# Optimization experiments

Hardware: AMD Instinct MI355X
Metric: run time of the kernel (lower is better)

The kernel has to match this reference:

```python
import jax, jax.numpy as jnp
import numpy as np

B, T, D = 4, 50, 512
SRC, SENTS, WORDS = 400, 16, 40
NEG = jnp.float32(-1e30)  # stands in for -inf mask fill (numerically identical post-softmax)


def _seq_mask(lengths, max_len):
    # [n, max_len] bool, True where position < length
    return jnp.arange(max_len)[None, :] < lengths[:, None]


def _mlp_score(q, h, Wq, bq, Uc, v):
    # Bahdanau additive score: v^T tanh(W q + U h)
    # q: [b,t,d], h: [b,s,d] -> [b,t,s]
    wq = q @ Wq + bq                       # [b,t,d]
    uh = h @ Uc                            # [b,s,d]
    wquh = jnp.tanh(wq[:, :, None, :] + uh[:, None, :, :])  # [b,t,s,d]
    return jnp.einsum('btsd,d->bts', wquh, v)


def setup_inputs() -> dict:
    key = jax.random.key(0)
    ks = jax.random.split(key, 20)
    s = np.float32(1.0 / np.sqrt(D))
    def p(k, shape):
        return jax.random.normal(k, shape, jnp.float32) * s
    return {
        'source': jax.random.normal(ks[0], (B, T, D), jnp.float32),
        'src_bank': jax.random.normal(ks[1], (SRC, B, D), jnp.float32),
        'src_lengths': jax.random.randint(ks[2], (B,), 1, SRC + 1),
        'qa_sent_bank': jax.random.normal(ks[3], (SENTS, B, D), jnp.float32),
        'qa_sent_lengths': jax.random.randint(ks[4], (B,), 1, SENTS + 1),
        'qa_word_bank': jax.random.normal(ks[5], (WORDS, B, SENTS, D), jnp.float32),
        'qa_word_lengths': jax.random.randint(ks[6], (B, SENTS), 1, WORDS + 1),
        'Wq_word': p(ks[7], (D, D)), 'bq_word': jnp.zeros((D,), jnp.float32),
        'Uc_word': p(ks[8], (D, D)), 'v_word': p(ks[9], (D,)),
        'Wq_sent': p(ks[10], (D, D)), 'bq_sent': jnp.zeros((D,), jnp.float32),
        'Uc_sent': p(ks[11], (D, D)), 'v_sent': p(ks[12], (D,)),
        'Wq_pass': p(ks[13], (D, D)), 'bq_pass': jnp.zeros((D,), jnp.float32),
        'Uc_pass': p(ks[14], (D, D)), 'v_pass': p(ks[15], (D,)),
    }


def _forward(source, src_bank, qa_sent_bank, qa_word_bank,
             Wq_word, bq_word, Uc_word, v_word,
             Wq_sent, bq_sent, Uc_sent, v_sent,
             Wq_pass, bq_pass, Uc_pass, v_pass,
             src_lengths, qa_word_lengths):
    b = source.shape[0]
    # [words,b,sents,d] -> [b,sents,words,d] -> [b, sents*words, d]
    qa_word = jnp.transpose(qa_word_bank, (1, 2, 0, 3)).reshape(b, SENTS * WORDS, D)
    src = jnp.transpose(src_bank, (1, 0, 2))       # [b,src,d]
    sent = jnp.transpose(qa_sent_bank, (1, 0, 2))  # [b,sents,d]

    qa_word_align = _mlp_score(source, qa_word, Wq_word, bq_word, Uc_word, v_word)  # [b,t,sents*words]
    src_align = _mlp_score(source, src, Wq_pass, bq_pass, Uc_pass, v_pass)          # [b,t,src]
    qa_sent_align = _mlp_score(source, sent, Wq_sent, bq_sent, Uc_sent, v_sent)     # [b,t,sents]

    # hierarchical combination: word score scaled by its sentence score
    qa_hier = (qa_word_align.reshape(b, T, SENTS, WORDS)
               * qa_sent_align[..., None]).reshape(b, T, SENTS * WORDS)

    align = jnp.concatenate([src_align, qa_hier], axis=-1)  # [b,t,src+sents*words]

    qa_mask = _seq_mask(qa_word_lengths.reshape(-1), WORDS).reshape(b, SENTS * WORDS)[:, None, :]
    src_mask = _seq_mask(src_lengths, SRC)[:, None, :]
    mask = jnp.concatenate([src_mask, qa_mask], axis=-1)

    align = jnp.where(mask, align, NEG)
    align_vectors = jax.nn.softmax(align, axis=-1)  # joint length-masked softmax

    memory = jnp.concatenate([src, qa_word], axis=1)          # [b, src+sents*words, d]
    c = jnp.einsum('bts,bsd->btd', align_vectors, memory)     # weighted context sum
    return c


def reference(source, src_bank, src_lengths, qa_sent_bank, qa_sent_lengths,
              qa_word_bank, qa_word_lengths,
              Wq_word, bq_word, Uc_word, v_word,
              Wq_sent, bq_sent, Uc_sent, v_sent,
              Wq_pass, bq_pass, Uc_pass, v_pass):
    # qa_sent_lengths is accepted but unused, matching the original forward()
    return _forward(source, src_bank, qa_sent_bank, qa_word_bank,
                    Wq_word, bq_word, Uc_word, v_word,
                    Wq_sent, bq_sent, Uc_sent, v_sent,
                    Wq_pass, bq_pass, Uc_pass, v_pass,
                    src_lengths, qa_word_lengths)
```

## Files before the change

### kernel.cpp

```cpp
#include <hip/hip_runtime.h>
#include <hip/hip_bf16.h>


#define B_    4
#define T_    50
#define D_    512
#define SRC_  400
#define SENTS_ 16
#define WORDS_ 40
#define NW_   640
#define NMEM_ 1040
#define NK_   1056
#define NJOB_ 1056

#define C2L2E 2.8853900817779268f

typedef unsigned short ushort_t;
using s8v = __attribute__((ext_vector_type(8))) short;
using f4v = __attribute__((ext_vector_type(4))) float;

#define OFF_WQ_WORD 0
#define OFF_WQ_SENT 102400
#define OFF_WQ_PASS 204800
#define OFF_UH_SRC  307200
#define OFF_UH_WORD 1126400
#define OFF_UH_SENT 2437120
#define OFF_SC_SRC  2469888
#define OFF_SC_WORD 2549888
#define OFF_SC_SENT 2677888
#define P_BYTE_OFF  10724352ull
#define MT_BYTE_OFF 11265024ull
#define WT_BYTE_OFF 15590400ull

__device__ __forceinline__ ushort_t f2b(float f) {
    __hip_bfloat16 h = __float2bfloat16(f);
    return *(ushort_t*)&h;
}

__global__ __launch_bounds__(256) void k0f_transpose(
    const float* __restrict__ w0, const float* __restrict__ w1,
    const float* __restrict__ w2, const float* __restrict__ w3,
    const float* __restrict__ w4, const float* __restrict__ w5,
    const float* __restrict__ src_bank, const float* __restrict__ qa_word_bank,
    ushort_t* __restrict__ wt, ushort_t* __restrict__ mt)
{
    __shared__ float tile[32][33];
    int bid = blockIdx.x;
    int tx = threadIdx.x & 31, ty = threadIdx.x >> 5;
    if (bid < 1536) {
        int z = bid >> 8, r = bid & 255;
        int n0 = (r & 15) * 32, k0 = (r >> 4) * 32;
        const float* W;
        switch (z) {
            case 0: W = w0; break; case 1: W = w1; break; case 2: W = w2; break;
            case 3: W = w3; break; case 4: W = w4; break; default: W = w5; break;
        }
        ushort_t* Wt = wt + z * (D_ * D_);
#pragma unroll
        for (int a = 0; a < 4; ++a)
            tile[ty + a * 8][tx] = W[(k0 + ty + a * 8) * D_ + n0 + tx];
        __syncthreads();
#pragma unroll
        for (int a = 0; a < 4; ++a)
            Wt[(n0 + ty + a * 8) * D_ + k0 + tx] = f2b(tile[tx][ty + a * 8]);
    } else {
        int tb = bid - 1536;
        int b = tb / 528, r = tb - b * 528;
        int s0 = (r % 33) * 32, d0 = (r / 33) * 32;
#pragma unroll
        for (int a = 0; a < 4; ++a) {
            int s = s0 + ty + a * 8;
            float val = 0.f;
            if (s < SRC_) {
                val = src_bank[(s * B_ + b) * D_ + d0 + tx];
            } else if (s < NMEM_) {
                int j = s - SRC_; int se = j / WORDS_; int wd = j - se * WORDS_;
                val = qa_word_bank[((wd * B_ + b) * SENTS_ + se) * D_ + d0 + tx];
            }
            tile[ty + a * 8][tx] = val;
        }
        __syncthreads();
        ushort_t* base = mt + (size_t)b * D_ * NK_;
#pragma unroll
        for (int a = 0; a < 4; ++a) {
            int d = d0 + ty + a * 8;
            base[(size_t)d * NK_ + s0 + tx] = f2b(tile[tx][ty + a * 8]);
        }
    }
}

__global__ __launch_bounds__(256) void k1_gemm(
    const float* __restrict__ source, const float* __restrict__ src_bank,
    const float* __restrict__ qa_sent_bank, const float* __restrict__ qa_word_bank,
    const ushort_t* __restrict__ wt,
    const float* __restrict__ bq_word, const float* __restrict__ bq_sent,
    const float* __restrict__ bq_pass,
    float* __restrict__ wsf)
{
    __shared__ short At[64 * 32];
    __shared__ short Bt[64 * 32];
    int bid = blockIdx.x;
    int z, rem;
    if (bid < 96)       { z = bid >> 5; rem = bid & 31; }
    else if (bid < 416) { z = 3; rem = bid - 96; }
    else if (bid < 616) { z = 4; rem = bid - 416; }
    else                { z = 5; rem = bid - 616; }
    int by = rem >> 3, bx = rem & 7;
    int M, atype; const float* bias; float* C;
    switch (z) {
        case 0: M = 200;  atype = 0; bias = bq_word; C = wsf + OFF_WQ_WORD; break;
        case 1: M = 200;  atype = 0; bias = bq_sent; C = wsf + OFF_WQ_SENT; break;
        case 2: M = 200;  atype = 0; bias = bq_pass; C = wsf + OFF_WQ_PASS; break;
        case 3: M = 2560; atype = 1; bias = nullptr; C = wsf + OFF_UH_WORD; break;
        case 4: M = 1600; atype = 2; bias = nullptr; C = wsf + OFF_UH_SRC;  break;
        default: M = 64;  atype = 3; bias = nullptr; C = wsf + OFF_UH_SENT; break;
    }
    int m0 = by * 64, n0 = bx * 64;
    const ushort_t* W = wt + z * (D_ * D_);

    int tid = threadIdx.x;
    int lane = tid & 63, wv = tid >> 6;
    int quad = lane >> 4, l16 = lane & 15;
    int sm = tid >> 2, koff = (tid & 3) * 8;

    const float* arow = nullptr;
    {
        int r = m0 + sm;
        if (r < M) {
            if (atype == 0) arow = source + r * D_;
            else if (atype == 1) { int b = r / NW_; int j = r - b * NW_;
                                   int se = j / WORDS_; int wd = j - se * WORDS_;
                                   arow = qa_word_bank + ((wd * B_ + b) * SENTS_ + se) * D_; }
            else if (atype == 2) { int b = r / SRC_; int j = r - b * SRC_;
                                   arow = src_bank + (j * B_ + b) * D_; }
            else                 { int b = r >> 4; int s2 = r & 15;
                                   arow = qa_sent_bank + (s2 * B_ + b) * D_; }
        }
    }
    const ushort_t* wrow = W + (n0 + sm) * D_;

    auto loadA = [&](float* r, int kk) {
        if (arow) {
            float4 f0 = *(const float4*)(arow + kk * 32 + koff);
            float4 f1 = *(const float4*)(arow + kk * 32 + koff + 4);
            r[0]=f0.x; r[1]=f0.y; r[2]=f0.z; r[3]=f0.w;
            r[4]=f1.x; r[5]=f1.y; r[6]=f1.z; r[7]=f1.w;
        } else {
#pragma unroll
            for (int i = 0; i < 8; ++i) r[i] = 0.f;
        }
    };

    f4v acc[4] = { {0.f,0.f,0.f,0.f}, {0.f,0.f,0.f,0.f},
                   {0.f,0.f,0.f,0.f}, {0.f,0.f,0.f,0.f} };

    float a0[8], a1[8];
    int4 w0v, w1v;
    loadA(a0, 0); w0v = *(const int4*)(wrow + 0 * 32 + koff);
    loadA(a1, 1); w1v = *(const int4*)(wrow + 1 * 32 + koff);

    for (int kk = 0; kk < 16; ++kk) {
        union { ushort_t u[8]; int4 v; } pk;
#pragma unroll
        for (int i = 0; i < 8; ++i) pk.u[i] = f2b(a0[i]);
        *(int4*)(At + sm * 32 + koff) = pk.v;
        *(int4*)(Bt + sm * 32 + koff) = w0v;
        __syncthreads();
#pragma unroll
        for (int i = 0; i < 8; ++i) a0[i] = a1[i];
        w0v = w1v;
        if (kk < 14) {
            loadA(a1, kk + 2);
            w1v = *(const int4*)(wrow + (kk + 2) * 32 + koff);
        }
        s8v af = *(const s8v*)(At + (wv * 16 + l16) * 32 + quad * 8);
#pragma unroll
        for (int ng = 0; ng < 4; ++ng) {
            s8v bf = *(const s8v*)(Bt + (ng * 16 + l16) * 32 + quad * 8);
            acc[ng] = __builtin_amdgcn_mfma_f32_16x16x32_bf16(af, bf, acc[ng], 0, 0, 0);
        }
        __syncthreads();
    }
#pragma unroll
    for (int ng = 0; ng < 4; ++ng) {
        int col = n0 + ng * 16 + l16;
        float bb = bias ? bias[col] : 0.f;
#pragma unroll
        for (int rr = 0; rr < 4; ++rr) {
            int row = m0 + wv * 16 + quad * 4 + rr;
            if (row < M) C[row * D_ + col] = (acc[ng][rr] + bb) * C2L2E;
        }
    }
}

__global__ __launch_bounds__(256) void k2_scores(
    const float* __restrict__ v_word, const float* __restrict__ v_sent,
    const float* __restrict__ v_pass,
    const int* __restrict__ src_lengths, const int* __restrict__ qa_word_lengths,
    float* __restrict__ wsf)
{
    int lane = threadIdx.x & 63;
    int jid = blockIdx.x * 4 + (threadIdx.x >> 6);
    int job = jid / 5, fifth = jid - job * 5;
    int b = job / NJOB_, slot = job - b * NJOB_;
    const float* uh; const float* v; const float* wq; float* out; int ostride;
    if (slot < SRC_) {
        if (slot >= src_lengths[b]) return;
        uh = wsf + OFF_UH_SRC + (size_t)(b * SRC_ + slot) * D_;
        v = v_pass; wq = wsf + OFF_WQ_PASS + b * T_ * D_;
        out = wsf + OFF_SC_SRC + b * T_ * SRC_ + slot; ostride = SRC_;
    } else if (slot < NMEM_) {
        int j = slot - SRC_;
        int se = j / WORDS_; int wd = j - se * WORDS_;
        if (wd >= qa_word_lengths[b * SENTS_ + se]) return;
        uh = wsf + OFF_UH_WORD + (size_t)(b * NW_ + j) * D_;
        v = v_word; wq = wsf + OFF_WQ_WORD + b * T_ * D_;
        out = wsf + OFF_SC_WORD + b * T_ * NW_ + j; ostride = NW_;
    } else {
        int s2 = slot - NMEM_;
        uh = wsf + OFF_UH_SENT + (size_t)(b * SENTS_ + s2) * D_;
        v = v_sent; wq = wsf + OFF_WQ_SENT + b * T_ * D_;
        out = wsf + OFF_SC_SENT + b * T_ * SENTS_ + s2; ostride = SENTS_;
    }
    int d0 = lane * 8;
    float4 u0 = *(const float4*)(uh + d0);
    float4 u1 = *(const float4*)(uh + d0 + 4);
    float uhr[8] = {u0.x, u0.y, u0.z, u0.w, u1.x, u1.y, u1.z, u1.w};
    float4 v0 = *(const float4*)(v + d0);
    float4 v1 = *(const float4*)(v + d0 + 4);
    float vr[8] = {v0.x, v0.y, v0.z, v0.w, v1.x, v1.y, v1.z, v1.w};

    float vs = ((vr[0] + vr[1]) + (vr[2] + vr[3])) + ((vr[4] + vr[5]) + (vr[6] + vr[7]));
#pragma unroll
    for (int off = 32; off > 0; off >>= 1) vs += __shfl_xor(vs, off, 64);

    const float* wqh = wq + (fifth * 10) * D_ + d0;
    int tbase = fifth * 10;
#pragma unroll 1
    for (int g = 0; g < 2; ++g) {
        float a5[5];
#pragma unroll
        for (int u5 = 0; u5 < 5; ++u5) {
            const float* wr = wqh + (g * 5 + u5) * D_;
            float4 w0 = *(const float4*)(wr);
            float4 w1 = *(const float4*)(wr + 4);
            float wrr[8] = {w0.x, w0.y, w0.z, w0.w, w1.x, w1.y, w1.z, w1.w};
            float a = 0.f;
#pragma unroll
            for (int j = 0; j < 8; ++j) {
                float e = __builtin_amdgcn_exp2f(wrr[j] + uhr[j]);
                float r = __builtin_amdgcn_rcpf(e + 1.f);
                a = fmaf(vr[j], r, a);
            }
            a5[u5] = a;
        }
#pragma unroll
        for (int off = 32; off > 0; off >>= 1) {
#pragma unroll
            for (int u5 = 0; u5 < 5; ++u5) a5[u5] += __shfl_xor(a5[u5], off, 64);
        }
        if (lane == 0) {
#pragma unroll
            for (int u5 = 0; u5 < 5; ++u5)
                out[(tbase + g * 5 + u5) * ostride] = fmaf(-2.f, a5[u5], vs);
        }
    }
}

__global__ __launch_bounds__(256) void k3a_softmax(
    const int* __restrict__ src_lengths, const int* __restrict__ qa_word_lengths,
    const float* __restrict__ wsf, ushort_t* __restrict__ P)
{
    __shared__ float p[NMEM_];
    __shared__ float red[4];
    int tid = threadIdx.x, lane = tid & 63, wv = tid >> 6;
    int bt = blockIdx.x, b = bt / T_, t = bt - b * T_;
    const float* sc_src  = wsf + OFF_SC_SRC  + bt * SRC_;
    const float* sc_word = wsf + OFF_SC_WORD + bt * NW_;
    const float* sc_sent = wsf + OFF_SC_SENT + bt * SENTS_;
    int slen = src_lengths[b];
    float mx = -3.0e38f;
    for (int j = tid; j < NMEM_; j += 256) {
        float val;
        if (j < SRC_) {
            val = (j < slen) ? sc_src[j] : -1e30f;
        } else {
            int jj = j - SRC_; int se = jj / WORDS_; int wd = jj - se * WORDS_;
            float raw = sc_word[jj] * sc_sent[se];
            val = (wd < qa_word_lengths[b * SENTS_ + se]) ? raw : -1e30f;
        }
        p[j] = val;
        mx = fmaxf(mx, val);
    }
#pragma unroll
    for (int off = 32; off > 0; off >>= 1) mx = fmaxf(mx, __shfl_xor(mx, off, 64));
    if (lane == 0) red[wv] = mx;
    __syncthreads();
    mx = fmaxf(fmaxf(red[0], red[1]), fmaxf(red[2], red[3]));
    __syncthreads();
    float lsum = 0.f;
    for (int j = tid; j < NMEM_; j += 256) {
        float e = __expf(p[j] - mx);
        p[j] = e; lsum += e;
    }
#pragma unroll
    for (int off = 32; off > 0; off >>= 1) lsum += __shfl_xor(lsum, off, 64);
    if (lane == 0) red[wv] = lsum;
    __syncthreads();
    float inv = 1.f / (red[0] + red[1] + red[2] + red[3]);
    ushort_t* prow = P + (size_t)(b * 64 + t) * NK_;
    for (int j = tid; j < NK_; j += 256)
        prow[j] = (j < NMEM_) ? f2b(p[j] * inv) : (ushort_t)0;
}

__global__ __launch_bounds__(256) void k3c_gemm(
    const ushort_t* __restrict__ P, const ushort_t* __restrict__ Mt,
    float* __restrict__ out)
{
    __shared__ short At[64 * 32];
    __shared__ short Bt[32 * 32];
    int b = blockIdx.y;
    int n0 = blockIdx.x * 32;
    int tid = threadIdx.x;
    int lane = tid & 63, wv = tid >> 6;
    int quad = lane >> 4, l16 = lane & 15;
    int smA = tid >> 2, koffA = (tid & 3) * 8;
    int smB = tid >> 3, koffB = (tid & 7) * 4;

    const ushort_t* arow = P + (size_t)(b * 64 + smA) * NK_ + koffA;
    const ushort_t* brow = Mt + ((size_t)(b * D_ + n0 + smB)) * NK_ + koffB;

    f4v acc[2] = { {0.f,0.f,0.f,0.f}, {0.f,0.f,0.f,0.f} };

    int4 a0 = *(const int4*)(arow);
    int2 b0 = *(const int2*)(brow);
    int4 a1 = *(const int4*)(arow + 32);
    int2 b1 = *(const int2*)(brow + 32);
    int4 a2 = *(const int4*)(arow + 64);
    int2 b2 = *(const int2*)(brow + 64);

    for (int kk = 0; kk < 33; ++kk) {
        *(int4*)(At + smA * 32 + koffA) = a0;
        *(int2*)(Bt + smB * 32 + koffB) = b0;
        __syncthreads();
        a0 = a1; a1 = a2; b0 = b1; b1 = b2;
        if (kk < 30) {
            a2 = *(const int4*)(arow + (kk + 3) * 32);
            b2 = *(const int2*)(brow + (kk + 3) * 32);
        }
        s8v af = *(const s8v*)(At + (wv * 16 + l16) * 32 + quad * 8);
#pragma unroll
        for (int ng = 0; ng < 2; ++ng) {
            s8v bf = *(const s8v*)(Bt + (ng * 16 + l16) * 32 + quad * 8);
            acc[ng] = __builtin_amdgcn_mfma_f32_16x16x32_bf16(af, bf, acc[ng], 0, 0, 0);
        }
        __syncthreads();
    }
#pragma unroll
    for (int ng = 0; ng < 2; ++ng) {
        int col = n0 + ng * 16 + l16;
#pragma unroll
        for (int rr = 0; rr < 4; ++rr) {
            int row = wv * 16 + quad * 4 + rr;
            if (row < T_) out[(size_t)(b * T_ + row) * D_ + col] = acc[ng][rr];
        }
    }
}

extern "C" void kernel_launch(void* const* d_in, const int* in_sizes, int n_in,
                              void* d_out, int out_size, void* d_ws, size_t ws_size,
                              hipStream_t stream)
{
    (void)in_sizes; (void)n_in; (void)out_size; (void)ws_size;
    const float* source          = (const float*)d_in[0];
    const float* src_bank        = (const float*)d_in[1];
    const int*   src_lengths     = (const int*)d_in[2];
    const float* qa_sent_bank    = (const float*)d_in[3];
    const float* qa_word_bank    = (const float*)d_in[5];
    const int*   qa_word_lengths = (const int*)d_in[6];
    const float* Wq_word = (const float*)d_in[7];
    const float* bq_word = (const float*)d_in[8];
    const float* Uc_word = (const float*)d_in[9];
    const float* v_word  = (const float*)d_in[10];
    const float* Wq_sent = (const float*)d_in[11];
    const float* bq_sent = (const float*)d_in[12];
    const float* Uc_sent = (const float*)d_in[13];
    const float* v_sent  = (const float*)d_in[14];
    const float* Wq_pass = (const float*)d_in[15];
    const float* bq_pass = (const float*)d_in[16];
    const float* Uc_pass = (const float*)d_in[17];
    const float* v_pass  = (const float*)d_in[18];

    float* wsf = (float*)d_ws;
    ushort_t* Pb  = (ushort_t*)((char*)d_ws + P_BYTE_OFF);
    ushort_t* mt  = (ushort_t*)((char*)d_ws + MT_BYTE_OFF);
    ushort_t* wt  = (ushort_t*)((char*)d_ws + WT_BYTE_OFF);
    float* out = (float*)d_out;

    k0f_transpose<<<dim3(3648), dim3(256), 0, stream>>>(
        Wq_word, Wq_sent, Wq_pass, Uc_word, Uc_pass, Uc_sent,
        src_bank, qa_word_bank, wt, mt);
    k1_gemm<<<dim3(624), dim3(256), 0, stream>>>(
        source, src_bank, qa_sent_bank, qa_word_bank, wt,
        bq_word, bq_sent, bq_pass, wsf);
    k2_scores<<<dim3(5280), dim3(256), 0, stream>>>(
        v_word, v_sent, v_pass, src_lengths, qa_word_lengths, wsf);
    k3a_softmax<<<dim3(200), dim3(256), 0, stream>>>(src_lengths, qa_word_lengths, wsf, Pb);
    k3c_gemm<<<dim3(16, 4), dim3(256), 0, stream>>>(Pb, mt, out);
}
```

Baseline: 153.0 us.

## Fuse weight transpose into projection GEMM and merge with memory transpose kernel

```diff
diff --git a/kernel.cpp b/kernel.cpp
--- a/kernel.cpp
+++ b/kernel.cpp
@@ -30,43 +30,32 @@
 #define OFF_SC_SENT 2677888
 #define P_BYTE_OFF  10724352ull
 #define MT_BYTE_OFF 11265024ull
-#define WT_BYTE_OFF 15590400ull
 
 __device__ __forceinline__ ushort_t f2b(float f) {
     __hip_bfloat16 h = __float2bfloat16(f);
     return *(ushort_t*)&h;
 }
 
-__global__ __launch_bounds__(256) void k0f_transpose(
+__global__ __launch_bounds__(256) void kA(
+    const float* __restrict__ source, const float* __restrict__ src_bank,
+    const float* __restrict__ qa_sent_bank, const float* __restrict__ qa_word_bank,
     const float* __restrict__ w0, const float* __restrict__ w1,
     const float* __restrict__ w2, const float* __restrict__ w3,
     const float* __restrict__ w4, const float* __restrict__ w5,
-    const float* __restrict__ src_bank, const float* __restrict__ qa_word_bank,
-    ushort_t* __restrict__ wt, ushort_t* __restrict__ mt)
+    const float* __restrict__ bq_word, const float* __restrict__ bq_sent,
+    const float* __restrict__ bq_pass,
+    float* __restrict__ wsf, ushort_t* __restrict__ mt)
 {
-    __shared__ float tile[32][33];
+    __shared__ float smemf[4224];
     int bid = blockIdx.x;
-    int tx = threadIdx.x & 31, ty = threadIdx.x >> 5;
-    if (bid < 1536) {
-        int z = bid >> 8, r = bid & 255;
-        int n0 = (r & 15) * 32, k0 = (r >> 4) * 32;
-        const float* W;
-        switch (z) {
-            case 0: W = w0; break; case 1: W = w1; break; case 2: W = w2; break;
-            case 3: W = w3; break; case 4: W = w4; break; default: W = w5; break;
-        }
-        ushort_t* Wt = wt + z * (D_ * D_);
-#pragma unroll
-        for (int a = 0; a < 4; ++a)
-            tile[ty + a * 8][tx] = W[(k0 + ty + a * 8) * D_ + n0 + tx];
-        __syncthreads();
-#pragma unroll
-        for (int a = 0; a < 4; ++a)
-            Wt[(n0 + ty + a * 8) * D_ + k0 + tx] = f2b(tile[tx][ty + a * 8]);
-    } else {
-        int tb = bid - 1536;
+    int tid = threadIdx.x;
+
+    if (bid >= 624) {
+        int tb = bid - 624;
         int b = tb / 528, r = tb - b * 528;
         int s0 = (r % 33) * 32, d0 = (r / 33) * 32;
+        float (*tile)[33] = (float(*)[33])smemf;
+        int tx = tid & 31, ty = tid >> 5;
 #pragma unroll
         for (int a = 0; a < 4; ++a) {
             int s = s0 + ty + a * 8;
@@ -86,58 +75,52 @@
             int d = d0 + ty + a * 8;
             base[(size_t)d * NK_ + s0 + tx] = f2b(tile[tx][ty + a * 8]);
         }
-    }
-}
-
-__global__ __launch_bounds__(256) void k1_gemm(
-    const float* __restrict__ source, const float* __restrict__ src_bank,
-    const float* __restrict__ qa_sent_bank, const float* __restrict__ qa_word_bank,
-    const ushort_t* __restrict__ wt,
-    const float* __restrict__ bq_word, const float* __restrict__ bq_sent,
-    const float* __restrict__ bq_pass,
-    float* __restrict__ wsf)
-{
-    __shared__ short At[64 * 32];
-    __shared__ short Bt[64 * 32];
-    int bid = blockIdx.x;
+        return;
+    }
+
     int z, rem;
     if (bid < 96)       { z = bid >> 5; rem = bid & 31; }
     else if (bid < 416) { z = 3; rem = bid - 96; }
     else if (bid < 616) { z = 4; rem = bid - 416; }
     else                { z = 5; rem = bid - 616; }
     int by = rem >> 3, bx = rem & 7;
-    int M, atype; const float* bias; float* C;
+    int M, atype; const float* bias; const float* W; float* C;
     switch (z) {
-        case 0: M = 200;  atype = 0; bias = bq_word; C = wsf + OFF_WQ_WORD; break;
-        case 1: M = 200;  atype = 0; bias = bq_sent; C = wsf + OFF_WQ_SENT; break;
-        case 2: M = 200;  atype = 0; bias = bq_pass; C = wsf + OFF_WQ_PASS; break;
-        case 3: M = 2560; atype = 1; bias = nullptr; C = wsf + OFF_UH_WORD; break;
-        case 4: M = 1600; atype = 2; bias = nullptr; C = wsf + OFF_UH_SRC;  break;
-        default: M = 64;  atype = 3; bias = nullptr; C = wsf + OFF_UH_SENT; break;
+        case 0: M = 200;  atype = 0; bias = bq_word; W = w0; C = wsf + OFF_WQ_WORD; break;
+        case 1: M = 200;  atype = 0; bias = bq_sent; W = w1; C = wsf + OFF_WQ_SENT; break;
+        case 2: M = 200;  atype = 0; bias = bq_pass; W = w2; C = wsf + OFF_WQ_PASS; break;
+        case 3: M = 2560; atype = 1; bias = nullptr; W = w3; C = wsf + OFF_UH_WORD; break;
+        case 4: M = 1600; atype = 2; bias = nullptr; W = w4; C = wsf + OFF_UH_SRC;  break;
+        default: M = 64;  atype = 3; bias = nullptr; W = w5; C = wsf + OFF_UH_SENT; break;
     }
     int m0 = by * 64, n0 = bx * 64;
-    const ushort_t* W = wt + z * (D_ * D_);
-
-    int tid = threadIdx.x;
-    int lane = tid & 63, wv = tid >> 6;
-    int quad = lane >> 4, l16 = lane & 15;
+
+    int lane = tid & 63, wvx = tid >> 6, quad = lane >> 4, l16 = lane & 15;
     int sm = tid >> 2, koff = (tid & 3) * 8;
+    int rW = tid >> 3, cW = (tid & 7) * 8;
+    int rWs = rW * 68 + (cW ^ (((rW >> 3) & 3) << 4));
+    int nB = tid >> 2, kB8 = (tid & 3) * 8;
+    int colp = nB ^ (((kB8 >> 3) & 3) << 4);
+
+    short* At = (short*)smemf;
+    short* Bt = (short*)(smemf + 1024);
+    float* Wtmp = smemf + 2048;
 
     const float* arow = nullptr;
     {
-        int r = m0 + sm;
-        if (r < M) {
-            if (atype == 0) arow = source + r * D_;
-            else if (atype == 1) { int b = r / NW_; int j = r - b * NW_;
+        int rr = m0 + sm;
+        if (rr < M) {
+            if (atype == 0) arow = source + rr * D_;
+            else if (atype == 1) { int b = rr / NW_; int j = rr - b * NW_;
                                    int se = j / WORDS_; int wd = j - se * WORDS_;
                                    arow = qa_word_bank + ((wd * B_ + b) * SENTS_ + se) * D_; }
-            else if (atype == 2) { int b = r / SRC_; int j = r - b * SRC_;
+            else if (atype == 2) { int b = rr / SRC_; int j = rr - b * SRC_;
                                    arow = src_bank + (j * B_ + b) * D_; }
-            else                 { int b = r >> 4; int s2 = r & 15;
+            else                 { int b = rr >> 4; int s2 = rr & 15;
                                    arow = qa_sent_bank + (s2 * B_ + b) * D_; }
         }
     }
-    const ushort_t* wrow = W + (n0 + sm) * D_;
+    const float* wbase = W + n0 + cW;
 
     auto loadA = [&](float* r, int kk) {
         if (arow) {
@@ -150,30 +133,56 @@
             for (int i = 0; i < 8; ++i) r[i] = 0.f;
         }
     };
+    auto loadW = [&](float* r, int kk) {
+        const float* p = wbase + (kk * 32 + rW) * D_;
+        float4 f0 = *(const float4*)p;
+        float4 f1 = *(const float4*)(p + 4);
+        r[0]=f0.x; r[1]=f0.y; r[2]=f0.z; r[3]=f0.w;
+        r[4]=f1.x; r[5]=f1.y; r[6]=f1.z; r[7]=f1.w;
+    };
+    auto storeWtmp = [&](const float* r) {
+        *(float4*)(Wtmp + rWs)     = float4{r[0], r[1], r[2], r[3]};
+        *(float4*)(Wtmp + rWs + 4) = float4{r[4], r[5], r[6], r[7]};
+    };
+    auto storeAt = [&](const float* r) {
+        union { ushort_t u[8]; int4 v; } pk;
+#pragma unroll
+        for (int i = 0; i < 8; ++i) pk.u[i] = f2b(r[i]);
+        *(int4*)(At + sm * 32 + koff) = pk.v;
+    };
+    auto buildBt = [&]() {
+        union { ushort_t u[8]; int4 v; } pk;
+#pragma unroll
+        for (int i = 0; i < 8; ++i) pk.u[i] = f2b(Wtmp[(kB8 + i) * 68 + colp]);
+        *(int4*)(Bt + nB * 32 + kB8) = pk.v;
+    };
 
     f4v acc[4] = { {0.f,0.f,0.f,0.f}, {0.f,0.f,0.f,0.f},
                    {0.f,0.f,0.f,0.f}, {0.f,0.f,0.f,0.f} };
 
-    float a0[8], a1[8];
-    int4 w0v, w1v;
-    loadA(a0, 0); w0v = *(const int4*)(wrow + 0 * 32 + koff);
-    loadA(a1, 1); w1v = *(const int4*)(wrow + 1 * 32 + koff);
+    float ac[8], an[8], wn[8];
+    loadA(ac, 0);
+    {
+        float w0r[8];
+        loadW(w0r, 0);
+        storeWtmp(w0r);
+    }
+    loadW(wn, 1);
+    loadA(an, 1);
+    __syncthreads();
 
     for (int kk = 0; kk < 16; ++kk) {
-        union { ushort_t u[8]; int4 v; } pk;
-#pragma unroll
-        for (int i = 0; i < 8; ++i) pk.u[i] = f2b(a0[i]);
-        *(int4*)(At + sm * 32 + koff) = pk.v;
-        *(int4*)(Bt + sm * 32 + koff) = w0v;
+        storeAt(ac);
+        buildBt();
         __syncthreads();
-#pragma unroll
-        for (int i = 0; i < 8; ++i) a0[i] = a1[i];
-        w0v = w1v;
-        if (kk < 14) {
-            loadA(a1, kk + 2);
-            w1v = *(const int4*)(wrow + (kk + 2) * 32 + koff);
-        }
-        s8v af = *(const s8v*)(At + (wv * 16 + l16) * 32 + quad * 8);
+        if (kk < 15) storeWtmp(wn);
+        if (kk < 14) loadW(wn, kk + 2);
+        if (kk < 15) {
+#pragma unroll
+            for (int i = 0; i < 8; ++i) ac[i] = an[i];
+        }
+        if (kk < 14) loadA(an, kk + 2);
+        s8v af = *(const s8v*)(At + (wvx * 16 + l16) * 32 + quad * 8);
 #pragma unroll
         for (int ng = 0; ng < 4; ++ng) {
             s8v bf = *(const s8v*)(Bt + (ng * 16 + l16) * 32 + quad * 8);
@@ -181,14 +190,15 @@
         }
         __syncthreads();
     }
+
 #pragma unroll
     for (int ng = 0; ng < 4; ++ng) {
         int col = n0 + ng * 16 + l16;
         float bb = bias ? bias[col] : 0.f;
 #pragma unroll
-        for (int rr = 0; rr < 4; ++rr) {
-            int row = m0 + wv * 16 + quad * 4 + rr;
-            if (row < M) C[row * D_ + col] = (acc[ng][rr] + bb) * C2L2E;
+        for (int rr2 = 0; rr2 < 4; ++rr2) {
+            int row = m0 + wvx * 16 + quad * 4 + rr2;
+            if (row < M) C[row * D_ + col] = (acc[ng][rr2] + bb) * C2L2E;
         }
     }
 }
@@ -394,15 +404,12 @@
     float* wsf = (float*)d_ws;
     ushort_t* Pb  = (ushort_t*)((char*)d_ws + P_BYTE_OFF);
     ushort_t* mt  = (ushort_t*)((char*)d_ws + MT_BYTE_OFF);
-    ushort_t* wt  = (ushort_t*)((char*)d_ws + WT_BYTE_OFF);
     float* out = (float*)d_out;
 
-    k0f_transpose<<<dim3(3648), dim3(256), 0, stream>>>(
+    kA<<<dim3(2736), dim3(256), 0, stream>>>(
+        source, src_bank, qa_sent_bank, qa_word_bank,
         Wq_word, Wq_sent, Wq_pass, Uc_word, Uc_pass, Uc_sent,
-        src_bank, qa_word_bank, wt, mt);
-    k1_gemm<<<dim3(624), dim3(256), 0, stream>>>(
-        source, src_bank, qa_sent_bank, qa_word_bank, wt,
-        bq_word, bq_sent, bq_pass, wsf);
+        bq_word, bq_sent, bq_pass, wsf, mt);
     k2_scores<<<dim3(5280), dim3(256), 0, stream>>>(
         v_word, v_sent, v_pass, src_lengths, qa_word_lengths, wsf);
     k3a_softmax<<<dim3(200), dim3(256), 0, stream>>>(src_lengths, qa_word_lengths, wsf, Pb);
```

Result: no change. 154.1 us (+0.7%).
